# Kernel optimization log

Hardware: AMD Instinct MI355X
Metric: run time of the kernel (lower is better)

## Reference

```python
import jax, jax.numpy as jnp
import numpy as np

N, E, C = 20000, 320000, 10000
IN, H, D = 768, 8, 64
HD = H * D
SA_H = 128


def _gat(feat, src, dst, W, al, ar, b):
    # DGL GATConv: fc -> per-node attn terms -> edge leaky_relu -> edge softmax over dst -> scatter-add -> bias -> elu
    h = (feat @ W).reshape(N, H, D)                       # [N,H,D]
    el = (h * al).sum(-1)                                 # [N,H]
    er = (h * ar).sum(-1)                                 # [N,H]
    e = jax.nn.leaky_relu(el[src] + er[dst], 0.2)         # [E,H]
    m = jax.ops.segment_max(e, dst, num_segments=N)       # [N,H]
    m = jnp.where(jnp.isfinite(m), m, 0.0)                # zero in-degree nodes
    ee = jnp.exp(e - m[dst])                              # [E,H]
    denom = jax.ops.segment_sum(ee, dst, num_segments=N)  # [N,H]
    a = ee / jnp.maximum(denom[dst], 1e-9)                # [E,H]
    out = jax.ops.segment_sum(a[:, :, None] * h[src], dst, num_segments=N)  # [N,H,D]
    return jax.nn.elu(out + b.reshape(1, H, D))


def _sem(z, w1, b1, w2):
    # SemanticAttention: per-metapath score -> softmax over metapaths -> weighted sum
    w = (jnp.tanh(z @ w1 + b1) @ w2).mean(0)              # [M,1]
    beta = jax.nn.softmax(w, axis=0)                      # [M,1]
    return (beta[None] * z).sum(1)                        # [C,HD]


def setup_inputs():
    key = jax.random.key(0)
    ks = jax.random.split(key, 32)
    inp = {}
    for i in range(3):
        inp[f"feat{i}"] = jax.random.normal(ks[i], (N, IN), jnp.float32)
        inp[f"src{i}"] = jax.random.randint(ks[3 + i], (E,), 0, N, dtype=jnp.int32)
        inp[f"dst{i}"] = jax.random.randint(ks[6 + i], (E,), 0, N, dtype=jnp.int32)
        inp[f"char{i}"] = jnp.arange(C, dtype=jnp.int32)
        inp[f"W{i}"] = jax.random.normal(ks[9 + i], (IN, HD), jnp.float32) * 0.05
        inp[f"al{i}"] = jax.random.normal(ks[12 + i], (H, D), jnp.float32) * 0.05
        inp[f"ar{i}"] = jax.random.normal(ks[15 + i], (H, D), jnp.float32) * 0.05
        inp[f"b{i}"] = jnp.zeros((HD,), jnp.float32)
    inp["sw1"] = jax.random.normal(ks[18], (HD, SA_H), jnp.float32) * 0.05
    inp["sb1"] = jnp.zeros((SA_H,), jnp.float32)
    inp["sw2"] = jax.random.normal(ks[19], (SA_H, 1), jnp.float32) * 0.05
    inp["aw1"] = jax.random.normal(ks[20], (HD, SA_H), jnp.float32) * 0.05
    inp["ab1"] = jnp.zeros((SA_H,), jnp.float32)
    inp["aw2"] = jax.random.normal(ks[21], (SA_H, 1), jnp.float32) * 0.05
    return inp


def reference(feat0, feat1, feat2, src0, src1, src2, dst0, dst1, dst2, char0, char1, char2,
              W0, W1, W2, al0, al1, al2, ar0, ar1, ar2, b0, b1, b2,
              sw1, sb1, sw2, aw1, ab1, aw2):
    h1 = _gat(feat0, src0, dst0, W0, al0, ar0, b0)        # [N,H,D]
    hh = _gat(feat2, src2, dst2, W2, al2, ar2, b2)        # [N,H,D]
    z = jnp.stack([h1[char0].reshape(C, HD), hh[char2].reshape(C, HD)], axis=1)  # [C,2,HD]
    sound = _sem(z, sw1, sb1, sw2)                        # [C,HD]
    h2 = _gat(feat1, src1, dst1, W1, al1, ar1, b1)        # [N,H,D]
    z2 = jnp.stack([sound, h2[char1].reshape(C, HD)], axis=1)  # [C,2,HD]
    sem_emb = _sem(z2, aw1, ab1, aw2).reshape(C, H, D)    # [C,H,D]
    h1 = h1.at[char0].set(sem_emb)
    h2 = h2.at[char1].set(sem_emb)
    hh = hh.at[char2].set(sem_emb)
    return sem_emb, h1.mean(1), h2.mean(1), hh.mean(1)
```

## Files before the change

kernel.cpp:

```cpp
#include <hip/hip_runtime.h>
#include <math.h>

#define NN 20000
#define NE 320000
#define CC 10000
#define KIN 768
#define NH 8
#define ND 64
#define NHD 512
#define NSA 128
#define NBKT 79

#define WTB_SZ (NHD * KIN)
#define W1TB_SZ (NSA * NHD)

typedef __attribute__((ext_vector_type(4))) float f32x4;
typedef __attribute__((ext_vector_type(8))) short s16x8;

__device__ __forceinline__ unsigned short f2bf(float f) {
  unsigned u = __float_as_uint(f);
  u += 0x7fffu + ((u >> 16) & 1u);
  return (unsigned short)(u >> 16);
}
__device__ __forceinline__ float bf2f(unsigned short s) {
  return __uint_as_float(((unsigned)s) << 16);
}
__device__ __forceinline__ float bflo(unsigned u) { return __uint_as_float(u << 16); }
__device__ __forceinline__ float bfhi(unsigned u) { return __uint_as_float(u & 0xffff0000u); }

__device__ __forceinline__ void gl_lds16(const void* g, void* l) {
  __builtin_amdgcn_global_load_lds(
      (const __attribute__((address_space(1))) unsigned int*)g,
      (__attribute__((address_space(3))) unsigned int*)l, 16, 0, 0);
}

__global__ void k_prep(const float* __restrict__ W0, const float* __restrict__ W1,
                       const float* __restrict__ W2, const float* __restrict__ sw1,
                       const float* __restrict__ aw1, unsigned short* __restrict__ wtb3,
                       unsigned short* __restrict__ w1tb2, int* __restrict__ deg3,
                       float* __restrict__ scal) {
  int i = blockIdx.x * 256 + threadIdx.x;
  if (i < 3 * WTB_SZ) {
    int g = i / WTB_SZ;
    int j = i - g * WTB_SZ;
    int n = j / KIN, k = j - n * KIN;
    const float* W = (g == 0) ? W0 : (g == 1) ? W1 : W2;
    wtb3[i] = f2bf(W[(size_t)k * NHD + n]);
    return;
  }
  i -= 3 * WTB_SZ;
  if (i < 2 * W1TB_SZ) {
    int p = i / W1TB_SZ;
    int j = i - p * W1TB_SZ;
    int n = j / NHD, k = j - n * NHD;
    const float* W = p ? aw1 : sw1;
    w1tb2[p * W1TB_SZ + n * NHD + k] = f2bf(W[(size_t)k * NSA + n]);
    return;
  }
  i -= 2 * W1TB_SZ;
  if (i < 3 * NN) { deg3[i] = 0; return; }
  i -= 3 * NN;
  if (i < 4) scal[i] = 0.f;
}

__global__ void k_cast_feat(const float* __restrict__ s, unsigned short* __restrict__ d, int n4) {
  int i = blockIdx.x * 256 + threadIdx.x;
  if (i >= n4) return;
  float4 v = ((const float4*)s)[i];
  ushort4 o;
  o.x = f2bf(v.x); o.y = f2bf(v.y); o.z = f2bf(v.z); o.w = f2bf(v.w);
  ((ushort4*)d)[i] = o;
}

__global__ __launch_bounds__(256, 2) void k_gemm_gat(const unsigned short* __restrict__ A,
                                                     const unsigned short* __restrict__ Bt,
                                                     unsigned short* __restrict__ outb,
                                                     const float* __restrict__ al,
                                                     const float* __restrict__ ar,
                                                     float* __restrict__ el,
                                                     float* __restrict__ er) {
  __shared__ unsigned short As[128 * 32];
  __shared__ unsigned short Bs[128 * 32];
  const int tid = threadIdx.x;
  const int wv = tid >> 6, lane = tid & 63;
  const int row0 = blockIdx.x * 128;
  const int col0 = blockIdx.y * 128;
  const int wr = (wv >> 1) * 64, wc = (wv & 1) * 64;
  const int ci = lane & 3, rsub = lane >> 2;

  f32x4 acc[4][4] = {};

  const int l15 = lane & 15;
  const int pc = (((lane >> 4) ^ ((l15 >> 1) & 3))) * 8;

  for (int k0 = 0; k0 < KIN; k0 += 32) {
#pragma unroll
    for (int i = 0; i < 2; i++) {
      int lrow = (wv * 2 + i) * 16 + rsub;
      int kc = (ci ^ ((lrow >> 1) & 3)) << 3;
      int ga = row0 + lrow; if (ga > NN - 1) ga = NN - 1;
      gl_lds16(A + (size_t)ga * KIN + k0 + kc, As + (wv * 2 + i) * 512);
      int gb = col0 + lrow;
      gl_lds16(Bt + (size_t)gb * KIN + k0 + kc, Bs + (wv * 2 + i) * 512);
    }
    __syncthreads();
    s16x8 af[4], bf[4];
#pragma unroll
    for (int m = 0; m < 4; m++) {
      af[m] = *(const s16x8*)(As + (wr + m * 16 + l15) * 32 + pc);
      bf[m] = *(const s16x8*)(Bs + (wc + m * 16 + l15) * 32 + pc);
    }
#pragma unroll
    for (int m = 0; m < 4; m++)
#pragma unroll
      for (int n = 0; n < 4; n++)
        acc[m][n] = __builtin_amdgcn_mfma_f32_16x16x32_bf16(af[m], bf[n], acc[m][n], 0, 0, 0);
    __syncthreads();
  }

  const int cbase = col0 + wc + l15;
  const int rq = (lane >> 4) * 4;
  const int hd = (col0 + wc) >> 6;
  float alc[4], arc[4];
#pragma unroll
  for (int n = 0; n < 4; n++) { alc[n] = al[cbase + n * 16]; arc[n] = ar[cbase + n * 16]; }

#pragma unroll
  for (int m = 0; m < 4; m++) {
#pragma unroll
    for (int r = 0; r < 4; r++) {
      int grow = row0 + wr + m * 16 + rq + r;
      float a = 0.f, b = 0.f;
#pragma unroll
      for (int n = 0; n < 4; n++) {
        float v = acc[m][n][r];
        a += v * alc[n];
        b += v * arc[n];
      }
      a += __shfl_xor(a, 1, 64); a += __shfl_xor(a, 2, 64);
      a += __shfl_xor(a, 4, 64); a += __shfl_xor(a, 8, 64);
      b += __shfl_xor(b, 1, 64); b += __shfl_xor(b, 2, 64);
      b += __shfl_xor(b, 4, 64); b += __shfl_xor(b, 8, 64);
      if (grow < NN) {
        unsigned short* dp = outb + (size_t)grow * NHD + cbase;
#pragma unroll
        for (int n = 0; n < 4; n++) dp[n * 16] = f2bf(acc[m][n][r]);
        if (l15 == 0) {
          el[(size_t)grow * NH + hd] = a;
          er[(size_t)grow * NH + hd] = b;
        }
      }
    }
  }
}

__global__ __launch_bounds__(256, 2) void k_gemm_sem(const unsigned short* __restrict__ A,
                                                     const unsigned short* __restrict__ Bt,
                                                     const float* __restrict__ b1,
                                                     const float* __restrict__ w2,
                                                     float* __restrict__ scal,
                                                     int M, int K) {
  __shared__ unsigned short As[128 * 32];
  __shared__ unsigned short Bs[128 * 32];
  __shared__ float rsum[2][128];
  __shared__ float pp[2][2];
  const int tid = threadIdx.x;
  const int wv = tid >> 6, lane = tid & 63;
  const int row0 = blockIdx.x * 128;
  const int wr = (wv >> 1) * 64, wc = (wv & 1) * 64;
  const int ci = lane & 3, rsub = lane >> 2;

  f32x4 acc[4][4] = {};

  const int l15 = lane & 15;
  const int pc = (((lane >> 4) ^ ((l15 >> 1) & 3))) * 8;

  for (int k0 = 0; k0 < K; k0 += 32) {
#pragma unroll
    for (int i = 0; i < 2; i++) {
      int lrow = (wv * 2 + i) * 16 + rsub;
      int kc = (ci ^ ((lrow >> 1) & 3)) << 3;
      int ga = row0 + lrow; if (ga > M - 1) ga = M - 1;
      gl_lds16(A + (size_t)ga * K + k0 + kc, As + (wv * 2 + i) * 512);
      int gb = lrow;
      gl_lds16(Bt + (size_t)gb * K + k0 + kc, Bs + (wv * 2 + i) * 512);
    }
    __syncthreads();
    s16x8 af[4], bf[4];
#pragma unroll
    for (int m = 0; m < 4; m++) {
      af[m] = *(const s16x8*)(As + (wr + m * 16 + l15) * 32 + pc);
      bf[m] = *(const s16x8*)(Bs + (wc + m * 16 + l15) * 32 + pc);
    }
#pragma unroll
    for (int m = 0; m < 4; m++)
#pragma unroll
      for (int n = 0; n < 4; n++)
        acc[m][n] = __builtin_amdgcn_mfma_f32_16x16x32_bf16(af[m], bf[n], acc[m][n], 0, 0, 0);
    __syncthreads();
  }

  if (tid < 128) { rsum[0][tid] = 0.f; rsum[1][tid] = 0.f; }
  __syncthreads();
  const int cb = wc + l15;
  const int rq = (lane >> 4) * 4;
  float b1c[4], w2c[4];
#pragma unroll
  for (int n = 0; n < 4; n++) { b1c[n] = b1[cb + n * 16]; w2c[n] = w2[cb + n * 16]; }
#pragma unroll
  for (int m = 0; m < 4; m++) {
#pragma unroll
    for (int r = 0; r < 4; r++) {
      int rl = wr + m * 16 + rq + r;
      float s = 0.f;
#pragma unroll
      for (int n = 0; n < 4; n++) s += tanhf(acc[m][n][r] + b1c[n]) * w2c[n];
      s += __shfl_xor(s, 1, 64); s += __shfl_xor(s, 2, 64);
      s += __shfl_xor(s, 4, 64); s += __shfl_xor(s, 8, 64);
      if (l15 == 0 && row0 + rl < M) rsum[wv & 1][rl] = s;
    }
  }
  __syncthreads();
  if (tid < 128) {
    int grow = row0 + tid;
    float v = rsum[0][tid] + rsum[1][tid];
    float vA = (grow < CC) ? v : 0.f;
    float vB = (grow >= CC && grow < M) ? v : 0.f;
#pragma unroll
    for (int off = 32; off > 0; off >>= 1) {
      vA += __shfl_xor(vA, off, 64);
      vB += __shfl_xor(vB, off, 64);
    }
    if ((tid & 63) == 0) { pp[tid >> 6][0] = vA; pp[tid >> 6][1] = vB; }
  }
  __syncthreads();
  if (tid == 0) {
    atomicAdd(scal + 0, pp[0][0] + pp[1][0]);
    atomicAdd(scal + 1, pp[0][1] + pp[1][1]);
  }
}

__global__ void k_hist3(const int* __restrict__ d0, const int* __restrict__ d1,
                        const int* __restrict__ d2, int* __restrict__ deg3) {
  int e = blockIdx.x * 256 + threadIdx.x;
  int g = blockIdx.y;
  const int* dst = (g == 0) ? d0 : (g == 1) ? d1 : d2;
  atomicAdd(deg3 + g * NN + dst[e], 1);
}

__global__ __launch_bounds__(1024) void k_scan3(const int* __restrict__ deg3,
                                                int* __restrict__ rowptr3,
                                                int* __restrict__ curB) {
  __shared__ int part[1024];
  const int g = blockIdx.x;
  const int* deg = deg3 + g * NN;
  int* rowptr = rowptr3 + g * (NN + 1);
  int tid = threadIdx.x;
  const int CH = 20;
  int base = tid * CH;
  int s = 0;
  for (int i = 0; i < CH; i++) { int idx = base + i; if (idx < NN) s += deg[idx]; }
  part[tid] = s;
  __syncthreads();
  for (int off = 1; off < 1024; off <<= 1) {
    int u = (tid >= off) ? part[tid - off] : 0;
    int v = part[tid];
    __syncthreads();
    part[tid] = u + v;
    __syncthreads();
  }
  int run = (tid == 0) ? 0 : part[tid - 1];
  for (int i = 0; i < CH; i++) {
    int idx = base + i;
    if (idx < NN) {
      rowptr[idx] = run;
      if ((idx & 255) == 0) curB[g * (NBKT + 1) + (idx >> 8)] = run;
      run += deg[idx];
    }
  }
  if (tid == 1023) rowptr[NN] = part[1023];
}

__global__ __launch_bounds__(1024) void k_coarse(const int* __restrict__ s0,
                                                 const int* __restrict__ s1,
                                                 const int* __restrict__ s2,
                                                 const int* __restrict__ d0,
                                                 const int* __restrict__ d1,
                                                 const int* __restrict__ d2,
                                                 int* __restrict__ curB,
                                                 unsigned* __restrict__ staging) {
  __shared__ int bcnt[NBKT];
  __shared__ int bbase[NBKT];
  int g = blockIdx.y;
  const int* src = (g == 0) ? s0 : (g == 1) ? s1 : s2;
  const int* dst = (g == 0) ? d0 : (g == 1) ? d1 : d2;
  int tid = threadIdx.x;
  if (tid < NBKT) bcnt[tid] = 0;
  __syncthreads();
  int e = blockIdx.x * 1024 + tid;
  bool val = e < NE;
  int b = 0, r = 0, sv = 0, dv = 0;
  if (val) {
    dv = dst[e]; sv = src[e];
    b = dv >> 8;
    r = atomicAdd(&bcnt[b], 1);
  }
  __syncthreads();
  if (tid < NBKT && bcnt[tid] > 0) bbase[tid] = atomicAdd(&curB[g * (NBKT + 1) + tid], bcnt[tid]);
  __syncthreads();
  if (val) staging[(size_t)g * NE + bbase[b] + r] = ((unsigned)sv << 8) | (unsigned)(dv & 255);
}

__global__ __launch_bounds__(1024) void k_fine(const int* __restrict__ rowptr3,
                                               const unsigned* __restrict__ staging,
                                               unsigned short* __restrict__ srcord3) {
  __shared__ int cur[256];
  int g = blockIdx.y, b = blockIdx.x;
  const int* rowptr = rowptr3 + g * (NN + 1);
  int n0 = b << 8;
  int tid = threadIdx.x;
  if (tid < 256) {
    int node = n0 + tid;
    cur[tid] = (node < NN) ? rowptr[node] : 0;
  }
  __syncthreads();
  int nend = n0 + 256; if (nend > NN) nend = NN;
  int start = rowptr[n0];
  int endp = rowptr[nend];
  for (int i = start + tid; i < endp; i += 1024) {
    unsigned u = staging[(size_t)g * NE + i];
    int nl = u & 255;
    int pos = atomicAdd(&cur[nl], 1);
    srcord3[(size_t)g * NE + pos] = (unsigned short)(u >> 8);
  }
}

__global__ __launch_bounds__(256) void k_aggf(const int* __restrict__ rowptr,
                                              const unsigned short* __restrict__ srcord,
                                              const float* __restrict__ el,
                                              const float* __restrict__ er,
                                              const unsigned short* __restrict__ hb,
                                              const float* __restrict__ bias,
                                              float* __restrict__ o,
                                              unsigned short* __restrict__ zb) {
  __shared__ float aS[4][64 * 8];
  __shared__ int sS[4][64];
  int wv = threadIdx.x >> 6;
  int t = (blockIdx.x * 256 + threadIdx.x) >> 6;
  int lane = threadIdx.x & 63;
  int h = lane >> 3;
  int beg = rowptr[t], end = rowptr[t + 1];

  float4 er0 = ((const float4*)(er + (size_t)t * NH))[0];
  float4 er1 = ((const float4*)(er + (size_t)t * NH))[1];
  float erow[8] = {er0.x, er0.y, er0.z, er0.w, er1.x, er1.y, er1.z, er1.w};

  float acc[8] = {0.f, 0.f, 0.f, 0.f, 0.f, 0.f, 0.f, 0.f};
  float den = 0.f;

  for (int cbeg = beg; cbeg < end; cbeg += 64) {
    int cnt = end - cbeg; if (cnt > 64) cnt = 64;
    bool valid = lane < cnt;
    int pidx = cbeg + lane; if (pidx > end - 1) pidx = end - 1;
    int s = srcord[pidx];
    if (valid) {
      sS[wv][lane] = s;
      float4 a0 = ((const float4*)(el + (size_t)s * NH))[0];
      float4 a1 = ((const float4*)(el + (size_t)s * NH))[1];
      float v[8] = {a0.x + erow[0], a0.y + erow[1], a0.z + erow[2], a0.w + erow[3],
                    a1.x + erow[4], a1.y + erow[5], a1.z + erow[6], a1.w + erow[7]};
#pragma unroll
      for (int k = 0; k < 8; k++) {
        float x = v[k];
        x = x >= 0.f ? x : 0.2f * x;
        aS[wv][lane * 8 + k] = __expf(x);
      }
    }
    const unsigned short* hbl = hb + lane * 8;
    int q = 0;
    for (; q + 1 < cnt; q += 2) {
      int s0 = sS[wv][q], s1 = sS[wv][q + 1];
      float w0 = aS[wv][q * 8 + h];
      float w1 = aS[wv][(q + 1) * 8 + h];
      uint4 v0 = *(const uint4*)(hbl + (size_t)s0 * NHD);
      uint4 v1 = *(const uint4*)(hbl + (size_t)s1 * NHD);
      den += w0 + w1;
      acc[0] += w0 * bflo(v0.x); acc[1] += w0 * bfhi(v0.x);
      acc[2] += w0 * bflo(v0.y); acc[3] += w0 * bfhi(v0.y);
      acc[4] += w0 * bflo(v0.z); acc[5] += w0 * bfhi(v0.z);
      acc[6] += w0 * bflo(v0.w); acc[7] += w0 * bfhi(v0.w);
      acc[0] += w1 * bflo(v1.x); acc[1] += w1 * bfhi(v1.x);
      acc[2] += w1 * bflo(v1.y); acc[3] += w1 * bfhi(v1.y);
      acc[4] += w1 * bflo(v1.z); acc[5] += w1 * bfhi(v1.z);
      acc[6] += w1 * bflo(v1.w); acc[7] += w1 * bfhi(v1.w);
    }
    if (q < cnt) {
      int s0 = sS[wv][q];
      float w0 = aS[wv][q * 8 + h];
      uint4 v0 = *(const uint4*)(hbl + (size_t)s0 * NHD);
      den += w0;
      acc[0] += w0 * bflo(v0.x); acc[1] += w0 * bfhi(v0.x);
      acc[2] += w0 * bflo(v0.y); acc[3] += w0 * bfhi(v0.y);
      acc[4] += w0 * bflo(v0.z); acc[5] += w0 * bfhi(v0.z);
      acc[6] += w0 * bflo(v0.w); acc[7] += w0 * bfhi(v0.w);
    }
  }

  float dn = 1.f / fmaxf(den, 1e-9f);
  float4 b0 = ((const float4*)(bias + lane * 8))[0];
  float4 b1 = ((const float4*)(bias + lane * 8))[1];
  float r[8];
  r[0] = acc[0] * dn + b0.x; r[1] = acc[1] * dn + b0.y;
  r[2] = acc[2] * dn + b0.z; r[3] = acc[3] * dn + b0.w;
  r[4] = acc[4] * dn + b1.x; r[5] = acc[5] * dn + b1.y;
  r[6] = acc[6] * dn + b1.z; r[7] = acc[7] * dn + b1.w;
#pragma unroll
  for (int j = 0; j < 8; j++) r[j] = r[j] > 0.f ? r[j] : expm1f(r[j]);
  float* op = o + (size_t)t * NHD + lane * 8;
  ((float4*)op)[0] = make_float4(r[0], r[1], r[2], r[3]);
  ((float4*)op)[1] = make_float4(r[4], r[5], r[6], r[7]);
  if (t < CC) {
    uint4 z;
    z.x = ((unsigned)f2bf(r[1]) << 16) | f2bf(r[0]);
    z.y = ((unsigned)f2bf(r[3]) << 16) | f2bf(r[2]);
    z.z = ((unsigned)f2bf(r[5]) << 16) | f2bf(r[4]);
    z.w = ((unsigned)f2bf(r[7]) << 16) | f2bf(r[6]);
    *(uint4*)(zb + (size_t)t * NHD + lane * 8) = z;
  }
}

__global__ void k_combine_s1(const float* __restrict__ scal, const float* __restrict__ zA,
                             const float* __restrict__ zB, unsigned short* __restrict__ outb) {
  int i = blockIdx.x * 256 + threadIdx.x;
  float w0 = scal[0] * (1.f / CC), w1v = scal[1] * (1.f / CC);
  float mx = fmaxf(w0, w1v);
  float e0 = expf(w0 - mx), e1 = expf(w1v - mx);
  float inv = 1.f / (e0 + e1);
  float b0 = e0 * inv, b1v = e1 * inv;
  float4 a = ((const float4*)zA)[i];
  float4 b = ((const float4*)zB)[i];
  ushort4 z;
  z.x = f2bf(b0 * a.x + b1v * b.x);
  z.y = f2bf(b0 * a.y + b1v * b.y);
  z.z = f2bf(b0 * a.z + b1v * b.z);
  z.w = f2bf(b0 * a.w + b1v * b.w);
  ((ushort4*)outb)[i] = z;
}

__global__ void k_comb2_means(const float* __restrict__ scal,
                              const unsigned short* __restrict__ zsound,
                              const float* __restrict__ o0, const float* __restrict__ o1,
                              const float* __restrict__ o2, float* __restrict__ outf,
                              float* __restrict__ m1, float* __restrict__ m2,
                              float* __restrict__ m3) {
  int idx = blockIdx.x * 256 + threadIdx.x;
  int n = idx >> 6, d = idx & 63;
  if (n < CC) {
    float w0 = scal[0] * (1.f / CC), w1v = scal[1] * (1.f / CC);
    float mx = fmaxf(w0, w1v);
    float e0 = expf(w0 - mx), e1 = expf(w1v - mx);
    float inv = 1.f / (e0 + e1);
    float b0 = e0 * inv, b1v = e1 * inv;
    const unsigned short* zs = zsound + (size_t)n * NHD + d;
    const float* p1 = o1 + (size_t)n * NHD + d;
    float* po = outf + (size_t)n * NHD + d;
    float v = 0.f;
#pragma unroll
    for (int h = 0; h < 8; h++) {
      float r = b0 * bf2f(zs[h * 64]) + b1v * p1[h * 64];
      po[h * 64] = r;
      v += r;
    }
    v *= 0.125f;
    m1[idx] = v; m2[idx] = v; m3[idx] = v;
  } else {
    const float* p0 = o0 + (size_t)n * NHD + d;
    const float* p1 = o1 + (size_t)n * NHD + d;
    const float* p2 = o2 + (size_t)n * NHD + d;
    float v0 = 0.f, v1 = 0.f, v2 = 0.f;
#pragma unroll
    for (int h = 0; h < 8; h++) { v0 += p0[h * 64]; v1 += p1[h * 64]; v2 += p2[h * 64]; }
    m1[idx] = v0 * 0.125f; m2[idx] = v1 * 0.125f; m3[idx] = v2 * 0.125f;
  }
}

extern "C" void kernel_launch(void* const* d_in, const int* in_sizes, int n_in,
                              void* d_out, int out_size, void* d_ws, size_t ws_size,
                              hipStream_t stream) {
  (void)in_sizes; (void)n_in; (void)out_size; (void)ws_size;

  const float* feat[3]; const int* srcp[3]; const int* dstp[3];
  const float* Wp[3]; const float* alp[3]; const float* arp[3]; const float* bp[3];
  for (int g = 0; g < 3; g++) {
    const int base = g * 8;
    feat[g] = (const float*)d_in[base + 0];
    srcp[g] = (const int*)d_in[base + 1];
    dstp[g] = (const int*)d_in[base + 2];
    Wp[g]   = (const float*)d_in[base + 4];
    alp[g]  = (const float*)d_in[base + 5];
    arp[g]  = (const float*)d_in[base + 6];
    bp[g]   = (const float*)d_in[base + 7];
  }
  const float* sw1 = (const float*)d_in[24];
  const float* sb1 = (const float*)d_in[25];
  const float* sw2 = (const float*)d_in[26];
  const float* aw1 = (const float*)d_in[27];
  const float* ab1 = (const float*)d_in[28];
  const float* aw2 = (const float*)d_in[29];

  char* wsp = (char*)d_ws;
  auto alloc = [&](size_t bytes) {
    char* p = wsp;
    wsp += (bytes + 255) & ~(size_t)255;
    return p;
  };
  float* o0 = (float*)alloc((size_t)NN * NHD * 4);
  float* o1 = (float*)alloc((size_t)NN * NHD * 4);
  float* o2 = (float*)alloc((size_t)NN * NHD * 4);
  unsigned short* hb = (unsigned short*)alloc((size_t)NN * NHD * 2);
  unsigned short* featb = (unsigned short*)alloc((size_t)NN * KIN * 2);
  unsigned short* wtb3 = (unsigned short*)alloc((size_t)3 * WTB_SZ * 2);
  unsigned short* w1tb2 = (unsigned short*)alloc((size_t)2 * W1TB_SZ * 2);
  unsigned short* zcat = (unsigned short*)alloc((size_t)2 * CC * NHD * 2);
  float* el = (float*)alloc((size_t)NN * NH * 4);
  float* er = (float*)alloc((size_t)NN * NH * 4);
  float* scal = (float*)alloc(256);
  int* deg3 = (int*)alloc((size_t)3 * NN * 4);
  int* rowptr3 = (int*)alloc((size_t)3 * (NN + 1) * 4 + 64);
  int* curB = (int*)alloc((size_t)3 * (NBKT + 1) * 4);
  unsigned* staging = (unsigned*)alloc((size_t)3 * NE * 4);
  unsigned short* srcord3 = (unsigned short*)alloc((size_t)3 * NE * 2);

  float* outf = (float*)d_out;
  float* outm1 = outf + (size_t)CC * NHD;
  float* outm2 = outm1 + (size_t)NN * ND;
  float* outm3 = outm2 + (size_t)NN * ND;

  const int PREP_T = 3 * WTB_SZ + 2 * W1TB_SZ + 3 * NN + 4;
  k_prep<<<(PREP_T + 255) / 256, 256, 0, stream>>>(Wp[0], Wp[1], Wp[2], sw1, aw1,
                                                   wtb3, w1tb2, deg3, scal);
  k_hist3<<<dim3(NE / 256, 3), 256, 0, stream>>>(dstp[0], dstp[1], dstp[2], deg3);
  k_scan3<<<3, 1024, 0, stream>>>(deg3, rowptr3, curB);
  k_coarse<<<dim3((NE + 1023) / 1024, 3), 1024, 0, stream>>>(
      srcp[0], srcp[1], srcp[2], dstp[0], dstp[1], dstp[2], curB, staging);
  k_fine<<<dim3(NBKT, 3), 1024, 0, stream>>>(rowptr3, staging, srcord3);

  auto gat = [&](int g, float* og, unsigned short* zb) {
    k_cast_feat<<<NN * KIN / 4 / 256, 256, 0, stream>>>(feat[g], featb, NN * KIN / 4);
    k_gemm_gat<<<dim3((NN + 127) / 128, NHD / 128), 256, 0, stream>>>(
        featb, wtb3 + (size_t)g * WTB_SZ, hb, alp[g], arp[g], el, er);
    k_aggf<<<NN * 64 / 256, 256, 0, stream>>>(rowptr3 + g * (NN + 1), srcord3 + (size_t)g * NE,
                                              el, er, hb, bp[g], og, zb);
  };

  gat(0, o0, zcat);
  gat(2, o2, zcat + (size_t)CC * NHD);

  k_gemm_sem<<<(2 * CC + 127) / 128, 256, 0, stream>>>(zcat, w1tb2, sb1, sw2, scal, 2 * CC, NHD);
  k_combine_s1<<<CC * NHD / 4 / 256, 256, 0, stream>>>(scal, o0, o2, zcat);

  gat(1, o1, zcat + (size_t)CC * NHD);

  k_gemm_sem<<<(2 * CC + 127) / 128, 256, 0, stream>>>(zcat, w1tb2 + W1TB_SZ, ab1, aw2,
                                                       scal + 2, 2 * CC, NHD);
  k_comb2_means<<<NN * 64 / 256, 256, 0, stream>>>(scal + 2, zcat, o0, o1, o2,
                                                   outf, outm1, outm2, outm3);
}
```

Baseline: 488.6 us.

## Store GAT outputs in bf16, batch feature casts, unroll aggregation by four

Result: faster. 460.2 us (-5.8%).

```diff
diff --git a/kernel.cpp b/kernel.cpp
--- a/kernel.cpp
+++ b/kernel.cpp
@@ -13,6 +13,7 @@
 
 #define WTB_SZ (NHD * KIN)
 #define W1TB_SZ (NSA * NHD)
+#define FEAT_SZ (NN * KIN)
 
 typedef __attribute__((ext_vector_type(4))) float f32x4;
 typedef __attribute__((ext_vector_type(8))) short s16x8;
@@ -63,13 +64,15 @@
   if (i < 4) scal[i] = 0.f;
 }
 
-__global__ void k_cast_feat(const float* __restrict__ s, unsigned short* __restrict__ d, int n4) {
+__global__ void k_cast_feat3(const float* __restrict__ f0, const float* __restrict__ f1,
+                             const float* __restrict__ f2, unsigned short* __restrict__ d3) {
   int i = blockIdx.x * 256 + threadIdx.x;
-  if (i >= n4) return;
+  int g = blockIdx.y;
+  const float* s = (g == 0) ? f0 : (g == 1) ? f1 : f2;
   float4 v = ((const float4*)s)[i];
   ushort4 o;
   o.x = f2bf(v.x); o.y = f2bf(v.y); o.z = f2bf(v.z); o.w = f2bf(v.w);
-  ((ushort4*)d)[i] = o;
+  ((ushort4*)(d3 + (size_t)g * FEAT_SZ))[i] = o;
 }
 
 __global__ __launch_bounds__(256, 2) void k_gemm_gat(const unsigned short* __restrict__ A,
@@ -154,16 +157,17 @@
   }
 }
 
-__global__ __launch_bounds__(256, 2) void k_gemm_sem(const unsigned short* __restrict__ A,
+__global__ __launch_bounds__(256, 2) void k_gemm_sem(const unsigned short* __restrict__ A0,
+                                                     const unsigned short* __restrict__ A1,
                                                      const unsigned short* __restrict__ Bt,
                                                      const float* __restrict__ b1,
                                                      const float* __restrict__ w2,
-                                                     float* __restrict__ scal,
-                                                     int M, int K) {
+                                                     float* __restrict__ scal) {
   __shared__ unsigned short As[128 * 32];
   __shared__ unsigned short Bs[128 * 32];
   __shared__ float rsum[2][128];
   __shared__ float pp[2][2];
+  const int M = 2 * CC;
   const int tid = threadIdx.x;
   const int wv = tid >> 6, lane = tid & 63;
   const int row0 = blockIdx.x * 128;
@@ -175,15 +179,17 @@
   const int l15 = lane & 15;
   const int pc = (((lane >> 4) ^ ((l15 >> 1) & 3))) * 8;
 
-  for (int k0 = 0; k0 < K; k0 += 32) {
+  for (int k0 = 0; k0 < NHD; k0 += 32) {
 #pragma unroll
     for (int i = 0; i < 2; i++) {
       int lrow = (wv * 2 + i) * 16 + rsub;
       int kc = (ci ^ ((lrow >> 1) & 3)) << 3;
       int ga = row0 + lrow; if (ga > M - 1) ga = M - 1;
-      gl_lds16(A + (size_t)ga * K + k0 + kc, As + (wv * 2 + i) * 512);
+      const unsigned short* Ap = (ga < CC) ? A0 + (size_t)ga * NHD
+                                           : A1 + (size_t)(ga - CC) * NHD;
+      gl_lds16(Ap + k0 + kc, As + (wv * 2 + i) * 512);
       int gb = lrow;
-      gl_lds16(Bt + (size_t)gb * K + k0 + kc, Bs + (wv * 2 + i) * 512);
+      gl_lds16(Bt + (size_t)gb * NHD + k0 + kc, Bs + (wv * 2 + i) * 512);
     }
     __syncthreads();
     s16x8 af[4], bf[4];
@@ -341,8 +347,7 @@
                                               const float* __restrict__ er,
                                               const unsigned short* __restrict__ hb,
                                               const float* __restrict__ bias,
-                                              float* __restrict__ o,
-                                              unsigned short* __restrict__ zb) {
+                                              unsigned short* __restrict__ ob) {
   __shared__ float aS[4][64 * 8];
   __shared__ int sS[4][64];
   int wv = threadIdx.x >> 6;
@@ -378,13 +383,17 @@
     }
     const unsigned short* hbl = hb + lane * 8;
     int q = 0;
-    for (; q + 1 < cnt; q += 2) {
-      int s0 = sS[wv][q], s1 = sS[wv][q + 1];
+    for (; q + 3 < cnt; q += 4) {
+      int s0 = sS[wv][q], s1 = sS[wv][q + 1], s2 = sS[wv][q + 2], s3 = sS[wv][q + 3];
       float w0 = aS[wv][q * 8 + h];
       float w1 = aS[wv][(q + 1) * 8 + h];
+      float w2 = aS[wv][(q + 2) * 8 + h];
+      float w3 = aS[wv][(q + 3) * 8 + h];
       uint4 v0 = *(const uint4*)(hbl + (size_t)s0 * NHD);
       uint4 v1 = *(const uint4*)(hbl + (size_t)s1 * NHD);
-      den += w0 + w1;
+      uint4 v2 = *(const uint4*)(hbl + (size_t)s2 * NHD);
+      uint4 v3 = *(const uint4*)(hbl + (size_t)s3 * NHD);
+      den += (w0 + w1) + (w2 + w3);
       acc[0] += w0 * bflo(v0.x); acc[1] += w0 * bfhi(v0.x);
       acc[2] += w0 * bflo(v0.y); acc[3] += w0 * bfhi(v0.y);
       acc[4] += w0 * bflo(v0.z); acc[5] += w0 * bfhi(v0.z);
@@ -393,8 +402,16 @@
       acc[2] += w1 * bflo(v1.y); acc[3] += w1 * bfhi(v1.y);
       acc[4] += w1 * bflo(v1.z); acc[5] += w1 * bfhi(v1.z);
       acc[6] += w1 * bflo(v1.w); acc[7] += w1 * bfhi(v1.w);
-    }
-    if (q < cnt) {
+      acc[0] += w2 * bflo(v2.x); acc[1] += w2 * bfhi(v2.x);
+      acc[2] += w2 * bflo(v2.y); acc[3] += w2 * bfhi(v2.y);
+      acc[4] += w2 * bflo(v2.z); acc[5] += w2 * bfhi(v2.z);
+      acc[6] += w2 * bflo(v2.w); acc[7] += w2 * bfhi(v2.w);
+      acc[0] += w3 * bflo(v3.x); acc[1] += w3 * bfhi(v3.x);
+      acc[2] += w3 * bflo(v3.y); acc[3] += w3 * bfhi(v3.y);
+      acc[4] += w3 * bflo(v3.z); acc[5] += w3 * bfhi(v3.z);
+      acc[6] += w3 * bflo(v3.w); acc[7] += w3 * bfhi(v3.w);
+    }
+    for (; q < cnt; q++) {
       int s0 = sS[wv][q];
       float w0 = aS[wv][q * 8 + h];
       uint4 v0 = *(const uint4*)(hbl + (size_t)s0 * NHD);
@@ -416,41 +433,40 @@
   r[6] = acc[6] * dn + b1.z; r[7] = acc[7] * dn + b1.w;
 #pragma unroll
   for (int j = 0; j < 8; j++) r[j] = r[j] > 0.f ? r[j] : expm1f(r[j]);
-  float* op = o + (size_t)t * NHD + lane * 8;
-  ((float4*)op)[0] = make_float4(r[0], r[1], r[2], r[3]);
-  ((float4*)op)[1] = make_float4(r[4], r[5], r[6], r[7]);
-  if (t < CC) {
-    uint4 z;
-    z.x = ((unsigned)f2bf(r[1]) << 16) | f2bf(r[0]);
-    z.y = ((unsigned)f2bf(r[3]) << 16) | f2bf(r[2]);
-    z.z = ((unsigned)f2bf(r[5]) << 16) | f2bf(r[4]);
-    z.w = ((unsigned)f2bf(r[7]) << 16) | f2bf(r[6]);
-    *(uint4*)(zb + (size_t)t * NHD + lane * 8) = z;
-  }
-}
-
-__global__ void k_combine_s1(const float* __restrict__ scal, const float* __restrict__ zA,
-                             const float* __restrict__ zB, unsigned short* __restrict__ outb) {
+  uint4 z;
+  z.x = ((unsigned)f2bf(r[1]) << 16) | f2bf(r[0]);
+  z.y = ((unsigned)f2bf(r[3]) << 16) | f2bf(r[2]);
+  z.z = ((unsigned)f2bf(r[5]) << 16) | f2bf(r[4]);
+  z.w = ((unsigned)f2bf(r[7]) << 16) | f2bf(r[6]);
+  *(uint4*)(ob + (size_t)t * NHD + lane * 8) = z;
+}
+
+__global__ void k_combine_s1(const float* __restrict__ scal,
+                             const unsigned short* __restrict__ zA,
+                             const unsigned short* __restrict__ zB,
+                             unsigned short* __restrict__ outb) {
   int i = blockIdx.x * 256 + threadIdx.x;
   float w0 = scal[0] * (1.f / CC), w1v = scal[1] * (1.f / CC);
   float mx = fmaxf(w0, w1v);
   float e0 = expf(w0 - mx), e1 = expf(w1v - mx);
   float inv = 1.f / (e0 + e1);
   float b0 = e0 * inv, b1v = e1 * inv;
-  float4 a = ((const float4*)zA)[i];
-  float4 b = ((const float4*)zB)[i];
+  ushort4 a = ((const ushort4*)zA)[i];
+  ushort4 b = ((const ushort4*)zB)[i];
   ushort4 z;
-  z.x = f2bf(b0 * a.x + b1v * b.x);
-  z.y = f2bf(b0 * a.y + b1v * b.y);
-  z.z = f2bf(b0 * a.z + b1v * b.z);
-  z.w = f2bf(b0 * a.w + b1v * b.w);
+  z.x = f2bf(b0 * bf2f(a.x) + b1v * bf2f(b.x));
+  z.y = f2bf(b0 * bf2f(a.y) + b1v * bf2f(b.y));
+  z.z = f2bf(b0 * bf2f(a.z) + b1v * bf2f(b.z));
+  z.w = f2bf(b0 * bf2f(a.w) + b1v * bf2f(b.w));
   ((ushort4*)outb)[i] = z;
 }
 
 __global__ void k_comb2_means(const float* __restrict__ scal,
                               const unsigned short* __restrict__ zsound,
-                              const float* __restrict__ o0, const float* __restrict__ o1,
-                              const float* __restrict__ o2, float* __restrict__ outf,
+                              const unsigned short* __restrict__ ob0,
+                              const unsigned short* __restrict__ ob1,
+                              const unsigned short* __restrict__ ob2,
+                              float* __restrict__ outf,
                               float* __restrict__ m1, float* __restrict__ m2,
                               float* __restrict__ m3) {
   int idx = blockIdx.x * 256 + threadIdx.x;
@@ -462,24 +478,26 @@
     float inv = 1.f / (e0 + e1);
     float b0 = e0 * inv, b1v = e1 * inv;
     const unsigned short* zs = zsound + (size_t)n * NHD + d;
-    const float* p1 = o1 + (size_t)n * NHD + d;
+    const unsigned short* p1 = ob1 + (size_t)n * NHD + d;
     float* po = outf + (size_t)n * NHD + d;
     float v = 0.f;
 #pragma unroll
     for (int h = 0; h < 8; h++) {
-      float r = b0 * bf2f(zs[h * 64]) + b1v * p1[h * 64];
+      float r = b0 * bf2f(zs[h * 64]) + b1v * bf2f(p1[h * 64]);
       po[h * 64] = r;
       v += r;
     }
     v *= 0.125f;
     m1[idx] = v; m2[idx] = v; m3[idx] = v;
   } else {
-    const float* p0 = o0 + (size_t)n * NHD + d;
-    const float* p1 = o1 + (size_t)n * NHD + d;
-    const float* p2 = o2 + (size_t)n * NHD + d;
+    const unsigned short* p0 = ob0 + (size_t)n * NHD + d;
+    const unsigned short* p1 = ob1 + (size_t)n * NHD + d;
+    const unsigned short* p2 = ob2 + (size_t)n * NHD + d;
     float v0 = 0.f, v1 = 0.f, v2 = 0.f;
 #pragma unroll
-    for (int h = 0; h < 8; h++) { v0 += p0[h * 64]; v1 += p1[h * 64]; v2 += p2[h * 64]; }
+    for (int h = 0; h < 8; h++) {
+      v0 += bf2f(p0[h * 64]); v1 += bf2f(p1[h * 64]); v2 += bf2f(p2[h * 64]);
+    }
     m1[idx] = v0 * 0.125f; m2[idx] = v1 * 0.125f; m3[idx] = v2 * 0.125f;
   }
 }
@@ -514,14 +532,14 @@
     wsp += (bytes + 255) & ~(size_t)255;
     return p;
   };
-  float* o0 = (float*)alloc((size_t)NN * NHD * 4);
-  float* o1 = (float*)alloc((size_t)NN * NHD * 4);
-  float* o2 = (float*)alloc((size_t)NN * NHD * 4);
+  unsigned short* ob0 = (unsigned short*)alloc((size_t)NN * NHD * 2);
+  unsigned short* ob1 = (unsigned short*)alloc((size_t)NN * NHD * 2);
+  unsigned short* ob2 = (unsigned short*)alloc((size_t)NN * NHD * 2);
   unsigned short* hb = (unsigned short*)alloc((size_t)NN * NHD * 2);
-  unsigned short* featb = (unsigned short*)alloc((size_t)NN * KIN * 2);
+  unsigned short* featb3 = (unsigned short*)alloc((size_t)3 * FEAT_SZ * 2);
   unsigned short* wtb3 = (unsigned short*)alloc((size_t)3 * WTB_SZ * 2);
   unsigned short* w1tb2 = (unsigned short*)alloc((size_t)2 * W1TB_SZ * 2);
-  unsigned short* zcat = (unsigned short*)alloc((size_t)2 * CC * NHD * 2);
+  unsigned short* sound = (unsigned short*)alloc((size_t)CC * NHD * 2);
   float* el = (float*)alloc((size_t)NN * NH * 4);
   float* er = (float*)alloc((size_t)NN * NH * 4);
   float* scal = (float*)alloc(256);
@@ -539,30 +557,29 @@
   const int PREP_T = 3 * WTB_SZ + 2 * W1TB_SZ + 3 * NN + 4;
   k_prep<<<(PREP_T + 255) / 256, 256, 0, stream>>>(Wp[0], Wp[1], Wp[2], sw1, aw1,
                                                    wtb3, w1tb2, deg3, scal);
+  k_cast_feat3<<<dim3(FEAT_SZ / 4 / 256, 3), 256, 0, stream>>>(feat[0], feat[1], feat[2], featb3);
   k_hist3<<<dim3(NE / 256, 3), 256, 0, stream>>>(dstp[0], dstp[1], dstp[2], deg3);
   k_scan3<<<3, 1024, 0, stream>>>(deg3, rowptr3, curB);
   k_coarse<<<dim3((NE + 1023) / 1024, 3), 1024, 0, stream>>>(
       srcp[0], srcp[1], srcp[2], dstp[0], dstp[1], dstp[2], curB, staging);
   k_fine<<<dim3(NBKT, 3), 1024, 0, stream>>>(rowptr3, staging, srcord3);
 
-  auto gat = [&](int g, float* og, unsigned short* zb) {
-    k_cast_feat<<<NN * KIN / 4 / 256, 256, 0, stream>>>(feat[g], featb, NN * KIN / 4);
+  auto gat = [&](int g, unsigned short* ob) {
     k_gemm_gat<<<dim3((NN + 127) / 128, NHD / 128), 256, 0, stream>>>(
-        featb, wtb3 + (size_t)g * WTB_SZ, hb, alp[g], arp[g], el, er);
+        featb3 + (size_t)g * FEAT_SZ, wtb3 + (size_t)g * WTB_SZ, hb, alp[g], arp[g], el, er);
     k_aggf<<<NN * 64 / 256, 256, 0, stream>>>(rowptr3 + g * (NN + 1), srcord3 + (size_t)g * NE,
-                                              el, er, hb, bp[g], og, zb);
+                                              el, er, hb, bp[g], ob);
   };
 
-  gat(0, o0, zcat);
-  gat(2, o2, zcat + (size_t)CC * NHD);
-
-  k_gemm_sem<<<(2 * CC + 127) / 128, 256, 0, stream>>>(zcat, w1tb2, sb1, sw2, scal, 2 * CC, NHD);
-  k_combine_s1<<<CC * NHD / 4 / 256, 256, 0, stream>>>(scal, o0, o2, zcat);
-
-  gat(1, o1, zcat + (size_t)CC * NHD);
-
-  k_gemm_sem<<<(2 * CC + 127) / 128, 256, 0, stream>>>(zcat, w1tb2 + W1TB_SZ, ab1, aw2,
-                                                       scal + 2, 2 * CC, NHD);
-  k_comb2_means<<<NN * 64 / 256, 256, 0, stream>>>(scal + 2, zcat, o0, o1, o2,
+  gat(0, ob0);
+  gat(2, ob2);
+
+  k_gemm_sem<<<(2 * CC + 127) / 128, 256, 0, stream>>>(ob0, ob2, w1tb2, sb1, sw2, scal);
+  k_combine_s1<<<CC * NHD / 4 / 256, 256, 0, stream>>>(scal, ob0, ob2, sound);
+
+  gat(1, ob1);
+
+  k_gemm_sem<<<(2 * CC + 127) / 128, 256, 0, stream>>>(sound, ob1, w1tb2 + W1TB_SZ, ab1, aw2, scal + 2);
+  k_comb2_means<<<NN * 64 / 256, 256, 0, stream>>>(scal + 2, sound, ob0, ob1, ob2,
                                                    outf, outm1, outm2, outm3);
 }
```
